# Kernel optimization log

Hardware: AMD Instinct MI355X
Metric: run time of the kernel (lower is better)

Reference implementation:

```python
import jax, jax.numpy as jnp
import numpy as np

SRC_LEN, TRG_LEN, BATCH, HID_DIM, ATT_DIM = 256, 256, 32, 512, 128


def setup_inputs() -> dict:
    key = jax.random.key(0)
    k1, k2, k3, k4, k5, k6 = jax.random.split(key, 6)
    dec_out = jax.random.normal(k1, (TRG_LEN, BATCH, HID_DIM), dtype=jnp.float32)
    enc_outs = jax.random.normal(k2, (SRC_LEN, BATCH, HID_DIM), dtype=jnp.float32)
    # Linear weights (scaled like kaiming-ish init so tanh isn't saturated)
    W_s = jax.random.normal(k3, (ATT_DIM, HID_DIM), dtype=jnp.float32) / np.sqrt(HID_DIM)
    W_t = jax.random.normal(k4, (ATT_DIM, HID_DIM), dtype=jnp.float32) / np.sqrt(HID_DIM)
    b_t = jax.random.normal(k5, (ATT_DIM,), dtype=jnp.float32) * 0.01
    # v_a ~ U(-0.05, 0.05), shape (att_dim, 1) as in the torch module
    v_a = jax.random.uniform(k6, (ATT_DIM, 1), dtype=jnp.float32, minval=-0.05, maxval=0.05)
    return {"dec_out": dec_out, "enc_outs": enc_outs, "W_s": W_s, "W_t": W_t, "b_t": b_t, "v_a": v_a}


def reference(dec_out, enc_outs, W_s, W_t, b_t, v_a):
    # enc projection: (src, batch, hid) -> (src, batch, att)
    enc_att = jnp.einsum('sbh,ah->sba', enc_outs, W_s)
    # dec projection (with bias): (trg, batch, hid) -> (trg, batch, att)
    dec_att = jnp.einsum('tbh,ah->tba', dec_out, W_t) + b_t
    # broadcast-add + tanh: (src, trg, batch, att), then reduce with v_a
    dec_enc = jnp.tanh(enc_att[:, None, :, :] + dec_att[None, :, :, :])
    scores = jnp.einsum('stba,a->tbs', dec_enc, v_a[:, 0])  # (trg, batch, src)
    return scores
```

## Files before the change

kernel.cpp:

```cpp
#include <hip/hip_runtime.h>

#define SRC_LEN 256
#define TRG_LEN 256
#define BATCH   32
#define HID     512
#define ATT     128
#define CSCALE  2.885390081777927f

typedef float  f32x4  __attribute__((ext_vector_type(4)));
typedef short  bf16x8 __attribute__((ext_vector_type(8)));

__device__ inline unsigned short bfr(float x) {
    unsigned u = __builtin_bit_cast(unsigned, x);
    return (unsigned short)((u + 0x7fffu + ((u >> 16) & 1u)) >> 16);
}
__device__ inline unsigned pk2(float a, float b) {
    return (unsigned)bfr(a) | ((unsigned)bfr(b) << 16);
}

__global__ __launch_bounds__(512) void proj_mfma(
    const float* __restrict__ dec_out, const float* __restrict__ enc_outs,
    const float* __restrict__ W_s, const float* __restrict__ W_t,
    const float* __restrict__ b_t,
    float* __restrict__ encE, float* __restrict__ decD)
{
    __shared__ __align__(16) char smem[49152];
    char* aLb = smem;
    char* bLb = smem + 16384;

    const int tid   = threadIdx.x;
    const int blk   = blockIdx.x;
    const bool isDec = blk >= 128;
    const int bb    = blk & 31;
    const int r0    = ((isDec ? blk - 128 : blk) >> 5) * 64;
    const float* __restrict__ in = isDec ? dec_out : enc_outs;
    const float* __restrict__ W  = isDec ? W_t : W_s;

    const int lane   = tid & 63;
    const int w      = tid >> 6;
    const int woff_m = (w & 3) * 16;
    const int woff_n = (w >> 2) * 64;
    const int q      = lane >> 4;
    const int l15    = lane & 15;
    const int l7     = lane & 7;

    const int srow = tid >> 4;
    const int skc  = tid & 15;
    const int sg   = skc >> 1, shalf = skc & 1;
    const float* aGp = in + ((size_t)(r0 + srow) * BATCH + bb) * HID + skc * 4;
    const float* wGp = W + (size_t)srow * HID + skc * 4;

    float4 aR[2];
    float4 wR[4];

    f32x4 acc[4];
    #pragma unroll
    for (int ni = 0; ni < 4; ++ni) acc[ni] = (f32x4)0.0f;

    #define LOADG(c)                                                          \
        {                                                                     \
            _Pragma("unroll")                                                 \
            for (int it = 0; it < 2; ++it)                                    \
                aR[it] = *(const float4*)(aGp + (size_t)it * 32 * BATCH * HID \
                                          + (c) * 64);                        \
            _Pragma("unroll")                                                 \
            for (int it = 0; it < 4; ++it)                                    \
                wR[it] = *(const float4*)(wGp + (size_t)it * 32 * HID         \
                                          + (c) * 64);                        \
        }

    #define STORES(buf)                                                      \
        {                                                                    \
            char* ab = aLb + (buf) * 8192;                                   \
            _Pragma("unroll")                                                \
            for (int it = 0; it < 2; ++it) {                                 \
                const int i = srow + it * 32;                                \
                uint2 u;                                                     \
                u.x = pk2(aR[it].x, aR[it].y);                               \
                u.y = pk2(aR[it].z, aR[it].w);                               \
                *(uint2*)(ab + i * 128 + ((sg ^ (i & 7)) << 4)               \
                          + shalf * 8) = u;                                  \
            }                                                                \
            char* bp = bLb + (buf) * 16384;                                  \
            _Pragma("unroll")                                                \
            for (int it = 0; it < 4; ++it) {                                 \
                const int rw = srow + it * 32;                               \
                uint2 u;                                                     \
                u.x = pk2(wR[it].x, wR[it].y);                               \
                u.y = pk2(wR[it].z, wR[it].w);                               \
                *(uint2*)(bp + rw * 128 + ((sg ^ (rw & 7)) << 4)             \
                          + shalf * 8) = u;                                  \
            }                                                                \
        }

    LOADG(0);
    STORES(0);
    __syncthreads();

    for (int c = 0; c < 8; ++c) {
        if (c < 7) LOADG(c + 1);
        const char* ab = aLb + (c & 1) * 8192;
        const char* bp = bLb + (c & 1) * 16384;
        #pragma unroll
        for (int s = 0; s < 2; ++s) {
            const int sw = ((s * 4 + q) ^ l7) * 16;
            bf16x8 af = *(const bf16x8*)(ab + (woff_m + l15) * 128 + sw);
            bf16x8 bfv[4];
            #pragma unroll
            for (int ni = 0; ni < 4; ++ni)
                bfv[ni] = *(const bf16x8*)(bp + (woff_n + ni * 16 + l15) * 128 + sw);
            #pragma unroll
            for (int ni = 0; ni < 4; ++ni)
                acc[ni] = __builtin_amdgcn_mfma_f32_16x16x32_bf16(
                    af, bfv[ni], acc[ni], 0, 0, 0);
        }
        if (c < 7) STORES((c + 1) & 1);
        __syncthreads();
    }

    if (!isDec) {
        float* T = (float*)smem;
        #pragma unroll
        for (int ni = 0; ni < 4; ++ni)
            #pragma unroll
            for (int r = 0; r < 4; ++r) {
                const int ml = woff_m + q * 4 + r;
                const int nl = woff_n + ni * 16 + l15;
                T[ml * 132 + nl] = __builtin_amdgcn_exp2f(-CSCALE * acc[ni][r]);
            }
        __syncthreads();
        {
            const int m  = tid & 63;
            const int g0 = tid >> 6;
            #pragma unroll
            for (int p = 0; p < 4; ++p) {
                const int gq = g0 + p * 8;
                float4 v = *(const float4*)(T + m * 132 + gq * 4);
                *(float4*)(encE + (((size_t)bb * 32 + gq) * SRC_LEN + r0 + m) * 4) = v;
            }
        }
    } else {
        float bt[4];
        #pragma unroll
        for (int ni = 0; ni < 4; ++ni) bt[ni] = b_t[woff_n + ni * 16 + l15];
        #pragma unroll
        for (int ni = 0; ni < 4; ++ni)
            #pragma unroll
            for (int r = 0; r < 4; ++r) {
                const int ml = woff_m + q * 4 + r;
                const int nl = woff_n + ni * 16 + l15;
                decD[((size_t)(r0 + ml) * BATCH + bb) * ATT + nl] =
                    __builtin_amdgcn_exp2f(CSCALE * (acc[ni][r] + bt[ni]));
            }
    }
    #undef LOADG
    #undef STORES
}

__global__ __launch_bounds__(256) void score_kernel(
    const float* __restrict__ encE, const float* __restrict__ decD,
    const float* __restrict__ v_a, float* __restrict__ out)
{
    __shared__ float dS[4 * ATT];
    __shared__ float vS[ATT];
    __shared__ float sumvS;

    const int tid = threadIdx.x;
    const int t0  = blockIdx.x * 4;
    const int b   = blockIdx.y;

    if (tid < 128) {
        const int tt = tid >> 5, a4 = (tid & 31) * 4;
        *(float4*)(dS + tt * ATT + a4) =
            *(const float4*)(decD + ((size_t)(t0 + tt) * BATCH + b) * ATT + a4);
    } else if (tid < 160) {
        const int l = tid - 128;
        *(float4*)(vS + l * 4) = *(const float4*)(v_a + l * 4);
    }
    __syncthreads();
    if (tid < 64) {
        float x = vS[tid] + vS[tid + 64];
        #pragma unroll
        for (int o = 32; o > 0; o >>= 1) x += __shfl_down(x, o);
        if (tid == 0) sumvS = x;
    }
    __syncthreads();

    float acc0 = 0.f, acc1 = 0.f, acc2 = 0.f, acc3 = 0.f;
    const float* __restrict__ ep = encE + ((size_t)b * 32 * SRC_LEN + tid) * 4;

    #pragma unroll
    for (int g = 0; g < 32; ++g) {
        const float4 E  = *(const float4*)(ep + (size_t)g * SRC_LEN * 4);
        const float4 vv = *(const float4*)(vS + g * 4);
        const float n0 = vv.x * E.x, n1 = vv.y * E.y;
        const float n2 = vv.z * E.z, n3 = vv.w * E.w;

        #define TSTEP(ACC, DBASE)                                          \
        {                                                                  \
            const float4 d = *(const float4*)(DBASE + g * 4);              \
            const float x0 = E.x + d.x, x1 = E.y + d.y;                    \
            const float x2 = E.z + d.z, x3 = E.w + d.w;                    \
            const float a01 = x0 * x1, a23 = x2 * x3;                      \
            const float den = a01 * a23;                                   \
            const float m01 = fmaf(n0, x1, n1 * x0);                       \
            const float m23 = fmaf(n2, x3, n3 * x2);                       \
            const float num = fmaf(m01, a23, m23 * a01);                   \
            ACC = fmaf(num, __builtin_amdgcn_rcpf(den), ACC);              \
        }
        TSTEP(acc0, dS + 0 * ATT)
        TSTEP(acc1, dS + 1 * ATT)
        TSTEP(acc2, dS + 2 * ATT)
        TSTEP(acc3, dS + 3 * ATT)
        #undef TSTEP
    }

    const float sv = sumvS;
    out[((size_t)(t0 + 0) * BATCH + b) * SRC_LEN + tid] = sv - 2.0f * acc0;
    out[((size_t)(t0 + 1) * BATCH + b) * SRC_LEN + tid] = sv - 2.0f * acc1;
    out[((size_t)(t0 + 2) * BATCH + b) * SRC_LEN + tid] = sv - 2.0f * acc2;
    out[((size_t)(t0 + 3) * BATCH + b) * SRC_LEN + tid] = sv - 2.0f * acc3;
}

extern "C" void kernel_launch(void* const* d_in, const int* in_sizes, int n_in,
                              void* d_out, int out_size, void* d_ws, size_t ws_size,
                              hipStream_t stream) {
    const float* dec_out  = (const float*)d_in[0];
    const float* enc_outs = (const float*)d_in[1];
    const float* W_s      = (const float*)d_in[2];
    const float* W_t      = (const float*)d_in[3];
    const float* b_t      = (const float*)d_in[4];
    const float* v_a      = (const float*)d_in[5];
    float* out = (float*)d_out;

    float* encE = (float*)d_ws;
    float* decD = encE + (size_t)BATCH * ATT * SRC_LEN;

    proj_mfma<<<256, 512, 0, stream>>>(dec_out, enc_outs, W_s, W_t, b_t, encE, decD);

    dim3 g3(TRG_LEN / 4, BATCH);
    score_kernel<<<g3, 256, 0, stream>>>(encE, decD, v_a, out);
}
```

Measured before the change: 116.5 us.

## Halve projection tiles, pack score math into float2, remap score grid

After: 118.5 us. No clear change (+1.7%).

```diff
diff --git a/kernel.cpp b/kernel.cpp
--- a/kernel.cpp
+++ b/kernel.cpp
@@ -8,6 +8,7 @@
 #define CSCALE  2.885390081777927f
 
 typedef float  f32x4  __attribute__((ext_vector_type(4)));
+typedef float  f32x2  __attribute__((ext_vector_type(2)));
 typedef short  bf16x8 __attribute__((ext_vector_type(8)));
 
 __device__ inline unsigned short bfr(float x) {
@@ -18,28 +19,29 @@
     return (unsigned)bfr(a) | ((unsigned)bfr(b) << 16);
 }
 
-__global__ __launch_bounds__(512) void proj_mfma(
+__global__ __launch_bounds__(512, 4) void proj_mfma(
     const float* __restrict__ dec_out, const float* __restrict__ enc_outs,
     const float* __restrict__ W_s, const float* __restrict__ W_t,
     const float* __restrict__ b_t,
     float* __restrict__ encE, float* __restrict__ decD)
 {
-    __shared__ __align__(16) char smem[49152];
+    __shared__ __align__(16) char smem[40960];
     char* aLb = smem;
-    char* bLb = smem + 16384;
+    char* bLb = smem + 8192;
 
     const int tid   = threadIdx.x;
     const int blk   = blockIdx.x;
-    const bool isDec = blk >= 128;
-    const int bb    = blk & 31;
-    const int r0    = ((isDec ? blk - 128 : blk) >> 5) * 64;
+    const bool isDec = blk >= 256;
+    const int blkL  = isDec ? blk - 256 : blk;
+    const int bb    = blkL & 31;
+    const int r0    = (blkL >> 5) * 32;
     const float* __restrict__ in = isDec ? dec_out : enc_outs;
     const float* __restrict__ W  = isDec ? W_t : W_s;
 
     const int lane   = tid & 63;
     const int w      = tid >> 6;
-    const int woff_m = (w & 3) * 16;
-    const int woff_n = (w >> 2) * 64;
+    const int woff_m = (w & 1) * 16;
+    const int woff_n = (w >> 1) * 32;
     const int q      = lane >> 4;
     const int l15    = lane & 15;
     const int l7     = lane & 7;
@@ -50,19 +52,16 @@
     const float* aGp = in + ((size_t)(r0 + srow) * BATCH + bb) * HID + skc * 4;
     const float* wGp = W + (size_t)srow * HID + skc * 4;
 
-    float4 aR[2];
+    float4 aR;
     float4 wR[4];
 
-    f32x4 acc[4];
-    #pragma unroll
-    for (int ni = 0; ni < 4; ++ni) acc[ni] = (f32x4)0.0f;
+    f32x4 acc[2];
+    acc[0] = (f32x4)0.0f;
+    acc[1] = (f32x4)0.0f;
 
     #define LOADG(c)                                                          \
         {                                                                     \
-            _Pragma("unroll")                                                 \
-            for (int it = 0; it < 2; ++it)                                    \
-                aR[it] = *(const float4*)(aGp + (size_t)it * 32 * BATCH * HID \
-                                          + (c) * 64);                        \
+            aR = *(const float4*)(aGp + (size_t)(c) * 64);                    \
             _Pragma("unroll")                                                 \
             for (int it = 0; it < 4; ++it)                                    \
                 wR[it] = *(const float4*)(wGp + (size_t)it * 32 * HID         \
@@ -71,13 +70,12 @@
 
     #define STORES(buf)                                                      \
         {                                                                    \
-            char* ab = aLb + (buf) * 8192;                                   \
-            _Pragma("unroll")                                                \
-            for (int it = 0; it < 2; ++it) {                                 \
-                const int i = srow + it * 32;                                \
+            char* ab = aLb + (buf) * 4096;                                   \
+            {                                                                \
+                const int i = srow;                                          \
                 uint2 u;                                                     \
-                u.x = pk2(aR[it].x, aR[it].y);                               \
-                u.y = pk2(aR[it].z, aR[it].w);                               \
+                u.x = pk2(aR.x, aR.y);                                       \
+                u.y = pk2(aR.z, aR.w);                                       \
                 *(uint2*)(ab + i * 128 + ((sg ^ (i & 7)) << 4)               \
                           + shalf * 8) = u;                                  \
             }                                                                \
@@ -99,18 +97,18 @@
 
     for (int c = 0; c < 8; ++c) {
         if (c < 7) LOADG(c + 1);
-        const char* ab = aLb + (c & 1) * 8192;
+        const char* ab = aLb + (c & 1) * 4096;
         const char* bp = bLb + (c & 1) * 16384;
         #pragma unroll
         for (int s = 0; s < 2; ++s) {
             const int sw = ((s * 4 + q) ^ l7) * 16;
             bf16x8 af = *(const bf16x8*)(ab + (woff_m + l15) * 128 + sw);
-            bf16x8 bfv[4];
-            #pragma unroll
-            for (int ni = 0; ni < 4; ++ni)
+            bf16x8 bfv[2];
+            #pragma unroll
+            for (int ni = 0; ni < 2; ++ni)
                 bfv[ni] = *(const bf16x8*)(bp + (woff_n + ni * 16 + l15) * 128 + sw);
             #pragma unroll
-            for (int ni = 0; ni < 4; ++ni)
+            for (int ni = 0; ni < 2; ++ni)
                 acc[ni] = __builtin_amdgcn_mfma_f32_16x16x32_bf16(
                     af, bfv[ni], acc[ni], 0, 0, 0);
         }
@@ -121,7 +119,7 @@
     if (!isDec) {
         float* T = (float*)smem;
         #pragma unroll
-        for (int ni = 0; ni < 4; ++ni)
+        for (int ni = 0; ni < 2; ++ni)
             #pragma unroll
             for (int r = 0; r < 4; ++r) {
                 const int ml = woff_m + q * 4 + r;
@@ -130,21 +128,21 @@
             }
         __syncthreads();
         {
-            const int m  = tid & 63;
-            const int g0 = tid >> 6;
-            #pragma unroll
-            for (int p = 0; p < 4; ++p) {
-                const int gq = g0 + p * 8;
+            const int m  = tid & 31;
+            const int g0 = tid >> 5;
+            #pragma unroll
+            for (int p = 0; p < 2; ++p) {
+                const int gq = g0 + p * 16;
                 float4 v = *(const float4*)(T + m * 132 + gq * 4);
                 *(float4*)(encE + (((size_t)bb * 32 + gq) * SRC_LEN + r0 + m) * 4) = v;
             }
         }
     } else {
-        float bt[4];
-        #pragma unroll
-        for (int ni = 0; ni < 4; ++ni) bt[ni] = b_t[woff_n + ni * 16 + l15];
-        #pragma unroll
-        for (int ni = 0; ni < 4; ++ni)
+        float bt[2];
+        bt[0] = b_t[woff_n + l15];
+        bt[1] = b_t[woff_n + 16 + l15];
+        #pragma unroll
+        for (int ni = 0; ni < 2; ++ni)
             #pragma unroll
             for (int r = 0; r < 4; ++r) {
                 const int ml = woff_m + q * 4 + r;
@@ -161,20 +159,26 @@
     const float* __restrict__ encE, const float* __restrict__ decD,
     const float* __restrict__ v_a, float* __restrict__ out)
 {
-    __shared__ float dS[4 * ATT];
+    __shared__ __align__(16) float dPf[2][ATT][2];
     __shared__ float vS[ATT];
     __shared__ float sumvS;
 
     const int tid = threadIdx.x;
-    const int t0  = blockIdx.x * 4;
-    const int b   = blockIdx.y;
-
-    if (tid < 128) {
-        const int tt = tid >> 5, a4 = (tid & 31) * 4;
-        *(float4*)(dS + tt * ATT + a4) =
-            *(const float4*)(decD + ((size_t)(t0 + tt) * BATCH + b) * ATT + a4);
-    } else if (tid < 160) {
-        const int l = tid - 128;
+    const int p   = blockIdx.x;
+    const int b   = (p & 7) * 4 + ((p >> 3) >> 6);
+    const int t0  = ((p >> 3) & 63) * 4;
+
+    if (tid < 64) {
+        const int pr = tid >> 5, a4 = (tid & 31) * 4;
+        const float4 dA = *(const float4*)(decD + ((size_t)(t0 + 2 * pr) * BATCH + b) * ATT + a4);
+        const float4 dB = *(const float4*)(decD + ((size_t)(t0 + 2 * pr + 1) * BATCH + b) * ATT + a4);
+        f32x2* dst = (f32x2*)&dPf[pr][a4][0];
+        dst[0] = (f32x2){dA.x, dB.x};
+        dst[1] = (f32x2){dA.y, dB.y};
+        dst[2] = (f32x2){dA.z, dB.z};
+        dst[3] = (f32x2){dA.w, dB.w};
+    } else if (tid < 96) {
+        const int l = tid - 64;
         *(float4*)(vS + l * 4) = *(const float4*)(v_a + l * 4);
     }
     __syncthreads();
@@ -186,40 +190,44 @@
     }
     __syncthreads();
 
-    float acc0 = 0.f, acc1 = 0.f, acc2 = 0.f, acc3 = 0.f;
+    f32x2 acc0 = {0.f, 0.f};
+    f32x2 acc1 = {0.f, 0.f};
     const float* __restrict__ ep = encE + ((size_t)b * 32 * SRC_LEN + tid) * 4;
+
+    #define PSTEP(ACC, PR)                                                 \
+    {                                                                      \
+        const f32x2* dp = (const f32x2*)&dPf[PR][g * 4][0];                \
+        const f32x2 x0 = e0 + dp[0], x1 = e1 + dp[1];                      \
+        const f32x2 x2 = e2 + dp[2], x3 = e3 + dp[3];                      \
+        const f32x2 a01 = x0 * x1, a23 = x2 * x3;                          \
+        const f32x2 den = a01 * a23;                                       \
+        const f32x2 m01 = n0 * x1 + n1 * x0;                               \
+        const f32x2 m23 = n2 * x3 + n3 * x2;                               \
+        const f32x2 num = m01 * a23 + m23 * a01;                           \
+        f32x2 r;                                                           \
+        r[0] = __builtin_amdgcn_rcpf(den[0]);                              \
+        r[1] = __builtin_amdgcn_rcpf(den[1]);                              \
+        ACC += num * r;                                                    \
+    }
 
     #pragma unroll
     for (int g = 0; g < 32; ++g) {
         const float4 E  = *(const float4*)(ep + (size_t)g * SRC_LEN * 4);
         const float4 vv = *(const float4*)(vS + g * 4);
-        const float n0 = vv.x * E.x, n1 = vv.y * E.y;
-        const float n2 = vv.z * E.z, n3 = vv.w * E.w;
-
-        #define TSTEP(ACC, DBASE)                                          \
-        {                                                                  \
-            const float4 d = *(const float4*)(DBASE + g * 4);              \
-            const float x0 = E.x + d.x, x1 = E.y + d.y;                    \
-            const float x2 = E.z + d.z, x3 = E.w + d.w;                    \
-            const float a01 = x0 * x1, a23 = x2 * x3;                      \
-            const float den = a01 * a23;                                   \
-            const float m01 = fmaf(n0, x1, n1 * x0);                       \
-            const float m23 = fmaf(n2, x3, n3 * x2);                       \
-            const float num = fmaf(m01, a23, m23 * a01);                   \
-            ACC = fmaf(num, __builtin_amdgcn_rcpf(den), ACC);              \
-        }
-        TSTEP(acc0, dS + 0 * ATT)
-        TSTEP(acc1, dS + 1 * ATT)
-        TSTEP(acc2, dS + 2 * ATT)
-        TSTEP(acc3, dS + 3 * ATT)
-        #undef TSTEP
-    }
+        const f32x2 e0 = {E.x, E.x}, e1 = {E.y, E.y};
+        const f32x2 e2 = {E.z, E.z}, e3 = {E.w, E.w};
+        const f32x2 n0 = vv.x * e0, n1 = vv.y * e1;
+        const f32x2 n2 = vv.z * e2, n3 = vv.w * e3;
+        PSTEP(acc0, 0)
+        PSTEP(acc1, 1)
+    }
+    #undef PSTEP
 
     const float sv = sumvS;
-    out[((size_t)(t0 + 0) * BATCH + b) * SRC_LEN + tid] = sv - 2.0f * acc0;
-    out[((size_t)(t0 + 1) * BATCH + b) * SRC_LEN + tid] = sv - 2.0f * acc1;
-    out[((size_t)(t0 + 2) * BATCH + b) * SRC_LEN + tid] = sv - 2.0f * acc2;
-    out[((size_t)(t0 + 3) * BATCH + b) * SRC_LEN + tid] = sv - 2.0f * acc3;
+    out[((size_t)(t0 + 0) * BATCH + b) * SRC_LEN + tid] = sv - 2.0f * acc0[0];
+    out[((size_t)(t0 + 1) * BATCH + b) * SRC_LEN + tid] = sv - 2.0f * acc0[1];
+    out[((size_t)(t0 + 2) * BATCH + b) * SRC_LEN + tid] = sv - 2.0f * acc1[0];
+    out[((size_t)(t0 + 3) * BATCH + b) * SRC_LEN + tid] = sv - 2.0f * acc1[1];
 }
 
 extern "C" void kernel_launch(void* const* d_in, const int* in_sizes, int n_in,
@@ -236,8 +244,7 @@
     float* encE = (float*)d_ws;
     float* decD = encE + (size_t)BATCH * ATT * SRC_LEN;
 
-    proj_mfma<<<256, 512, 0, stream>>>(dec_out, enc_outs, W_s, W_t, b_t, encE, decD);
-
-    dim3 g3(TRG_LEN / 4, BATCH);
-    score_kernel<<<g3, 256, 0, stream>>>(encE, decD, v_a, out);
-}
+    proj_mfma<<<512, 512, 0, stream>>>(dec_out, enc_outs, W_s, W_t, b_t, encE, decD);
+
+    score_kernel<<<2048, 256, 0, stream>>>(encE, decD, v_a, out);
+}
```

## Prepack bf16 weights in a prep kernel and shrink projection tiles

Applied to the files above, without the earlier changes.

New measurement: 123.1 us. 1.06x slower.

```diff
diff --git a/kernel.cpp b/kernel.cpp
--- a/kernel.cpp
+++ b/kernel.cpp
@@ -18,79 +18,81 @@
     return (unsigned)bfr(a) | ((unsigned)bfr(b) << 16);
 }
 
-__global__ __launch_bounds__(512) void proj_mfma(
+__global__ __launch_bounds__(256) void prep_kernel(
+    const float* __restrict__ W_s, const float* __restrict__ W_t,
+    const float* __restrict__ v_a,
+    uint4* __restrict__ Wb, float* __restrict__ sumvP)
+{
+    const int blk = blockIdx.x;
+    if (blk < 16) {
+        const int iw = blk >> 3, a_tile = blk & 7;
+        const float* __restrict__ W = iw ? W_t : W_s;
+        uint4* __restrict__ dst = Wb + ((size_t)iw * 8 + a_tile) * 1024;
+        #pragma unroll
+        for (int oo = 0; oo < 4; ++oo) {
+            const int o = threadIdx.x + oo * 256;
+            const int c = o >> 7, rem = o & 127;
+            const int s = rem >> 6, lane = rem & 63;
+            const int q = lane >> 4, l15 = lane & 15;
+            const int row = a_tile * 16 + l15;
+            const int k0 = c * 64 + s * 32 + q * 8;
+            const float4 f0 = *(const float4*)(W + (size_t)row * HID + k0);
+            const float4 f1 = *(const float4*)(W + (size_t)row * HID + k0 + 4);
+            uint4 u;
+            u.x = pk2(f0.x, f0.y); u.y = pk2(f0.z, f0.w);
+            u.z = pk2(f1.x, f1.y); u.w = pk2(f1.z, f1.w);
+            dst[o] = u;
+        }
+    } else {
+        const int tid = threadIdx.x;
+        float x = 0.f;
+        if (tid < 64) x = v_a[tid] + v_a[tid + 64];
+        #pragma unroll
+        for (int o = 32; o > 0; o >>= 1) x += __shfl_down(x, o);
+        if (tid == 0) *sumvP = x;
+    }
+}
+
+__global__ __launch_bounds__(256, 4) void proj_mfma(
     const float* __restrict__ dec_out, const float* __restrict__ enc_outs,
-    const float* __restrict__ W_s, const float* __restrict__ W_t,
-    const float* __restrict__ b_t,
+    const float* __restrict__ b_t, const uint4* __restrict__ Wb,
     float* __restrict__ encE, float* __restrict__ decD)
 {
-    __shared__ __align__(16) char smem[49152];
-    char* aLb = smem;
-    char* bLb = smem + 16384;
+    __shared__ __align__(16) char smem[8704];
 
     const int tid   = threadIdx.x;
     const int blk   = blockIdx.x;
-    const bool isDec = blk >= 128;
-    const int bb    = blk & 31;
-    const int r0    = ((isDec ? blk - 128 : blk) >> 5) * 64;
+    const bool isDec = blk >= 512;
+    const int blkL  = isDec ? blk - 512 : blk;
+    const int bb    = blkL & 31;
+    const int r0    = (blkL >> 5) * 16;
     const float* __restrict__ in = isDec ? dec_out : enc_outs;
-    const float* __restrict__ W  = isDec ? W_t : W_s;
-
-    const int lane   = tid & 63;
-    const int w      = tid >> 6;
-    const int woff_m = (w & 3) * 16;
-    const int woff_n = (w >> 2) * 64;
-    const int q      = lane >> 4;
-    const int l15    = lane & 15;
-    const int l7     = lane & 7;
+    const uint4* __restrict__ Wk = Wb + (isDec ? 8192 : 0);
+
+    const int lane = tid & 63;
+    const int w    = tid >> 6;
+    const int woff_n = w * 32;
+    const int q = lane >> 4, l15 = lane & 15, l7 = lane & 7;
 
     const int srow = tid >> 4;
     const int skc  = tid & 15;
     const int sg   = skc >> 1, shalf = skc & 1;
     const float* aGp = in + ((size_t)(r0 + srow) * BATCH + bb) * HID + skc * 4;
-    const float* wGp = W + (size_t)srow * HID + skc * 4;
-
-    float4 aR[2];
-    float4 wR[4];
-
-    f32x4 acc[4];
-    #pragma unroll
-    for (int ni = 0; ni < 4; ++ni) acc[ni] = (f32x4)0.0f;
-
-    #define LOADG(c)                                                          \
-        {                                                                     \
-            _Pragma("unroll")                                                 \
-            for (int it = 0; it < 2; ++it)                                    \
-                aR[it] = *(const float4*)(aGp + (size_t)it * 32 * BATCH * HID \
-                                          + (c) * 64);                        \
-            _Pragma("unroll")                                                 \
-            for (int it = 0; it < 4; ++it)                                    \
-                wR[it] = *(const float4*)(wGp + (size_t)it * 32 * HID         \
-                                          + (c) * 64);                        \
-        }
-
+
+    float4 aR;
+    f32x4 acc[2];
+    acc[0] = (f32x4)0.0f;
+    acc[1] = (f32x4)0.0f;
+
+    #define LOADG(c) { aR = *(const float4*)(aGp + (size_t)(c) * 64); }
     #define STORES(buf)                                                      \
         {                                                                    \
-            char* ab = aLb + (buf) * 8192;                                   \
-            _Pragma("unroll")                                                \
-            for (int it = 0; it < 2; ++it) {                                 \
-                const int i = srow + it * 32;                                \
-                uint2 u;                                                     \
-                u.x = pk2(aR[it].x, aR[it].y);                               \
-                u.y = pk2(aR[it].z, aR[it].w);                               \
-                *(uint2*)(ab + i * 128 + ((sg ^ (i & 7)) << 4)               \
-                          + shalf * 8) = u;                                  \
-            }                                                                \
-            char* bp = bLb + (buf) * 16384;                                  \
-            _Pragma("unroll")                                                \
-            for (int it = 0; it < 4; ++it) {                                 \
-                const int rw = srow + it * 32;                               \
-                uint2 u;                                                     \
-                u.x = pk2(wR[it].x, wR[it].y);                               \
-                u.y = pk2(wR[it].z, wR[it].w);                               \
-                *(uint2*)(bp + rw * 128 + ((sg ^ (rw & 7)) << 4)             \
-                          + shalf * 8) = u;                                  \
-            }                                                                \
+            char* ab = smem + (buf) * 2048;                                  \
+            uint2 u;                                                         \
+            u.x = pk2(aR.x, aR.y);                                           \
+            u.y = pk2(aR.z, aR.w);                                           \
+            *(uint2*)(ab + srow * 128 + ((sg ^ (srow & 7)) << 4)             \
+                      + shalf * 8) = u;                                      \
         }
 
     LOADG(0);
@@ -99,20 +101,18 @@
 
     for (int c = 0; c < 8; ++c) {
         if (c < 7) LOADG(c + 1);
-        const char* ab = aLb + (c & 1) * 8192;
-        const char* bp = bLb + (c & 1) * 16384;
+        const char* ab = smem + (c & 1) * 2048;
         #pragma unroll
         for (int s = 0; s < 2; ++s) {
-            const int sw = ((s * 4 + q) ^ l7) * 16;
-            bf16x8 af = *(const bf16x8*)(ab + (woff_m + l15) * 128 + sw);
-            bf16x8 bfv[4];
-            #pragma unroll
-            for (int ni = 0; ni < 4; ++ni)
-                bfv[ni] = *(const bf16x8*)(bp + (woff_n + ni * 16 + l15) * 128 + sw);
-            #pragma unroll
-            for (int ni = 0; ni < 4; ++ni)
+            bf16x8 af = *(const bf16x8*)(ab + l15 * 128
+                                         + (((s * 4 + q) ^ l7) << 4));
+            #pragma unroll
+            for (int ni = 0; ni < 2; ++ni) {
+                const int a_tile = w * 2 + ni;
+                bf16x8 bfv = *(const bf16x8*)(Wk + (((a_tile * 8 + c) * 2 + s) * 64 + lane));
                 acc[ni] = __builtin_amdgcn_mfma_f32_16x16x32_bf16(
-                    af, bfv[ni], acc[ni], 0, 0, 0);
+                    af, bfv, acc[ni], 0, 0, 0);
+            }
         }
         if (c < 7) STORES((c + 1) & 1);
         __syncthreads();
@@ -121,33 +121,33 @@
     if (!isDec) {
         float* T = (float*)smem;
         #pragma unroll
-        for (int ni = 0; ni < 4; ++ni)
+        for (int ni = 0; ni < 2; ++ni)
             #pragma unroll
             for (int r = 0; r < 4; ++r) {
-                const int ml = woff_m + q * 4 + r;
+                const int ml = q * 4 + r;
                 const int nl = woff_n + ni * 16 + l15;
                 T[ml * 132 + nl] = __builtin_amdgcn_exp2f(-CSCALE * acc[ni][r]);
             }
         __syncthreads();
         {
-            const int m  = tid & 63;
-            const int g0 = tid >> 6;
-            #pragma unroll
-            for (int p = 0; p < 4; ++p) {
-                const int gq = g0 + p * 8;
+            const int m  = tid & 15;
+            const int g0 = tid >> 4;
+            #pragma unroll
+            for (int p = 0; p < 2; ++p) {
+                const int gq = g0 + p * 16;
                 float4 v = *(const float4*)(T + m * 132 + gq * 4);
                 *(float4*)(encE + (((size_t)bb * 32 + gq) * SRC_LEN + r0 + m) * 4) = v;
             }
         }
     } else {
-        float bt[4];
-        #pragma unroll
-        for (int ni = 0; ni < 4; ++ni) bt[ni] = b_t[woff_n + ni * 16 + l15];
-        #pragma unroll
-        for (int ni = 0; ni < 4; ++ni)
+        float bt[2];
+        bt[0] = b_t[woff_n + l15];
+        bt[1] = b_t[woff_n + 16 + l15];
+        #pragma unroll
+        for (int ni = 0; ni < 2; ++ni)
             #pragma unroll
             for (int r = 0; r < 4; ++r) {
-                const int ml = woff_m + q * 4 + r;
+                const int ml = q * 4 + r;
                 const int nl = woff_n + ni * 16 + l15;
                 decD[((size_t)(r0 + ml) * BATCH + bb) * ATT + nl] =
                     __builtin_amdgcn_exp2f(CSCALE * (acc[ni][r] + bt[ni]));
@@ -159,46 +159,28 @@
 
 __global__ __launch_bounds__(256) void score_kernel(
     const float* __restrict__ encE, const float* __restrict__ decD,
-    const float* __restrict__ v_a, float* __restrict__ out)
+    const float* __restrict__ v_a, const float* __restrict__ sumvP,
+    float* __restrict__ out)
 {
-    __shared__ float dS[4 * ATT];
-    __shared__ float vS[ATT];
-    __shared__ float sumvS;
-
     const int tid = threadIdx.x;
     const int t0  = blockIdx.x * 4;
     const int b   = blockIdx.y;
 
-    if (tid < 128) {
-        const int tt = tid >> 5, a4 = (tid & 31) * 4;
-        *(float4*)(dS + tt * ATT + a4) =
-            *(const float4*)(decD + ((size_t)(t0 + tt) * BATCH + b) * ATT + a4);
-    } else if (tid < 160) {
-        const int l = tid - 128;
-        *(float4*)(vS + l * 4) = *(const float4*)(v_a + l * 4);
-    }
-    __syncthreads();
-    if (tid < 64) {
-        float x = vS[tid] + vS[tid + 64];
-        #pragma unroll
-        for (int o = 32; o > 0; o >>= 1) x += __shfl_down(x, o);
-        if (tid == 0) sumvS = x;
-    }
-    __syncthreads();
-
     float acc0 = 0.f, acc1 = 0.f, acc2 = 0.f, acc3 = 0.f;
     const float* __restrict__ ep = encE + ((size_t)b * 32 * SRC_LEN + tid) * 4;
+    const float* __restrict__ dBase = decD + ((size_t)t0 * BATCH + b) * ATT;
 
     #pragma unroll
     for (int g = 0; g < 32; ++g) {
         const float4 E  = *(const float4*)(ep + (size_t)g * SRC_LEN * 4);
-        const float4 vv = *(const float4*)(vS + g * 4);
+        const float4 vv = *(const float4*)(v_a + g * 4);
         const float n0 = vv.x * E.x, n1 = vv.y * E.y;
         const float n2 = vv.z * E.z, n3 = vv.w * E.w;
 
-        #define TSTEP(ACC, DBASE)                                          \
+        #define TSTEP(ACC, TT)                                             \
         {                                                                  \
-            const float4 d = *(const float4*)(DBASE + g * 4);              \
+            const float4 d = *(const float4*)(dBase                        \
+                + (size_t)(TT) * BATCH * ATT + g * 4);         \
             const float x0 = E.x + d.x, x1 = E.y + d.y;                    \
             const float x2 = E.z + d.z, x3 = E.w + d.w;                    \
             const float a01 = x0 * x1, a23 = x2 * x3;                      \
@@ -208,14 +190,14 @@
             const float num = fmaf(m01, a23, m23 * a01);                   \
             ACC = fmaf(num, __builtin_amdgcn_rcpf(den), ACC);              \
         }
-        TSTEP(acc0, dS + 0 * ATT)
-        TSTEP(acc1, dS + 1 * ATT)
-        TSTEP(acc2, dS + 2 * ATT)
-        TSTEP(acc3, dS + 3 * ATT)
+        TSTEP(acc0, 0)
+        TSTEP(acc1, 1)
+        TSTEP(acc2, 2)
+        TSTEP(acc3, 3)
         #undef TSTEP
     }
 
-    const float sv = sumvS;
+    const float sv = *sumvP;
     out[((size_t)(t0 + 0) * BATCH + b) * SRC_LEN + tid] = sv - 2.0f * acc0;
     out[((size_t)(t0 + 1) * BATCH + b) * SRC_LEN + tid] = sv - 2.0f * acc1;
     out[((size_t)(t0 + 2) * BATCH + b) * SRC_LEN + tid] = sv - 2.0f * acc2;
@@ -235,9 +217,10 @@
 
     float* encE = (float*)d_ws;
     float* decD = encE + (size_t)BATCH * ATT * SRC_LEN;
-
-    proj_mfma<<<256, 512, 0, stream>>>(dec_out, enc_outs, W_s, W_t, b_t, encE, decD);
-
-    dim3 g3(TRG_LEN / 4, BATCH);
-    score_kernel<<<g3, 256, 0, stream>>>(encE, decD, v_a, out);
-}
+    uint4* Wb   = (uint4*)(decD + (size_t)TRG_LEN * BATCH * ATT);
+    float* sumvP = (float*)(Wb + 2 * 8192);
+
+    prep_kernel<<<17, 256, 0, stream>>>(W_s, W_t, v_a, Wb, sumvP);
+    proj_mfma<<<1024, 256, 0, stream>>>(dec_out, enc_outs, b_t, Wb, encE, decD);
+    score_kernel<<<dim3(TRG_LEN / 4, BATCH), 256, 0, stream>>>(encE, decD, v_a, sumvP, out);
+}
```

## Register-tile score kernel over 4 sources x 4 targets per thread

Applied to the files above, without the earlier changes.

New measurement: 128.2 us. 10.1% more time.

```diff
diff --git a/kernel.cpp b/kernel.cpp
--- a/kernel.cpp
+++ b/kernel.cpp
@@ -161,22 +161,25 @@
     const float* __restrict__ encE, const float* __restrict__ decD,
     const float* __restrict__ v_a, float* __restrict__ out)
 {
-    __shared__ float dS[4 * ATT];
+    __shared__ __align__(16) float dS[16][ATT];
     __shared__ float vS[ATT];
     __shared__ float sumvS;
 
     const int tid = threadIdx.x;
-    const int t0  = blockIdx.x * 4;
+    const int t0  = blockIdx.x * 16;
     const int b   = blockIdx.y;
 
-    if (tid < 128) {
-        const int tt = tid >> 5, a4 = (tid & 31) * 4;
-        *(float4*)(dS + tt * ATT + a4) =
-            *(const float4*)(decD + ((size_t)(t0 + tt) * BATCH + b) * ATT + a4);
-    } else if (tid < 160) {
-        const int l = tid - 128;
-        *(float4*)(vS + l * 4) = *(const float4*)(v_a + l * 4);
-    }
+    {
+        const int tr0 = tid >> 5;
+        const int a4  = (tid & 31) * 4;
+        #pragma unroll
+        for (int p = 0; p < 2; ++p) {
+            const int tr = tr0 + p * 8;
+            *(float4*)(&dS[tr][a4]) =
+                *(const float4*)(decD + ((size_t)(t0 + tr) * BATCH + b) * ATT + a4);
+        }
+    }
+    if (tid < 32) *(float4*)(vS + tid * 4) = *(const float4*)(v_a + tid * 4);
     __syncthreads();
     if (tid < 64) {
         float x = vS[tid] + vS[tid + 64];
@@ -186,40 +189,57 @@
     }
     __syncthreads();
 
-    float acc0 = 0.f, acc1 = 0.f, acc2 = 0.f, acc3 = 0.f;
-    const float* __restrict__ ep = encE + ((size_t)b * 32 * SRC_LEN + tid) * 4;
-
+    const int w  = tid >> 6;
+    const int l  = tid & 63;
+    const int s0 = l * 4;
+
+    f32x4 acc[4];
     #pragma unroll
+    for (int i = 0; i < 4; ++i) acc[i] = (f32x4)0.0f;
+
+    const float* __restrict__ ep = encE + (size_t)b * 32 * SRC_LEN * 4 + s0 * 4;
+
+    #pragma unroll 4
     for (int g = 0; g < 32; ++g) {
-        const float4 E  = *(const float4*)(ep + (size_t)g * SRC_LEN * 4);
+        const float* epg = ep + (size_t)g * SRC_LEN * 4;
+        float4 E[4];
+        #pragma unroll
+        for (int si = 0; si < 4; ++si)
+            E[si] = *(const float4*)(epg + si * 4);
         const float4 vv = *(const float4*)(vS + g * 4);
-        const float n0 = vv.x * E.x, n1 = vv.y * E.y;
-        const float n2 = vv.z * E.z, n3 = vv.w * E.w;
-
-        #define TSTEP(ACC, DBASE)                                          \
-        {                                                                  \
-            const float4 d = *(const float4*)(DBASE + g * 4);              \
-            const float x0 = E.x + d.x, x1 = E.y + d.y;                    \
-            const float x2 = E.z + d.z, x3 = E.w + d.w;                    \
-            const float a01 = x0 * x1, a23 = x2 * x3;                      \
-            const float den = a01 * a23;                                   \
-            const float m01 = fmaf(n0, x1, n1 * x0);                       \
-            const float m23 = fmaf(n2, x3, n3 * x2);                       \
-            const float num = fmaf(m01, a23, m23 * a01);                   \
-            ACC = fmaf(num, __builtin_amdgcn_rcpf(den), ACC);              \
-        }
-        TSTEP(acc0, dS + 0 * ATT)
-        TSTEP(acc1, dS + 1 * ATT)
-        TSTEP(acc2, dS + 2 * ATT)
-        TSTEP(acc3, dS + 3 * ATT)
-        #undef TSTEP
+        float4 n[4];
+        #pragma unroll
+        for (int si = 0; si < 4; ++si) {
+            n[si].x = vv.x * E[si].x; n[si].y = vv.y * E[si].y;
+            n[si].z = vv.z * E[si].z; n[si].w = vv.w * E[si].w;
+        }
+        #pragma unroll
+        for (int i = 0; i < 4; ++i) {
+            const float4 d = *(const float4*)(&dS[w * 4 + i][g * 4]);
+            #pragma unroll
+            for (int si = 0; si < 4; ++si) {
+                const float x0 = E[si].x + d.x, x1 = E[si].y + d.y;
+                const float x2 = E[si].z + d.z, x3 = E[si].w + d.w;
+                const float a01 = x0 * x1, a23 = x2 * x3;
+                const float den = a01 * a23;
+                const float m01 = fmaf(n[si].x, x1, n[si].y * x0);
+                const float m23 = fmaf(n[si].z, x3, n[si].w * x2);
+                const float num = fmaf(m01, a23, m23 * a01);
+                acc[i][si] = fmaf(num, __builtin_amdgcn_rcpf(den), acc[i][si]);
+            }
+        }
     }
 
     const float sv = sumvS;
-    out[((size_t)(t0 + 0) * BATCH + b) * SRC_LEN + tid] = sv - 2.0f * acc0;
-    out[((size_t)(t0 + 1) * BATCH + b) * SRC_LEN + tid] = sv - 2.0f * acc1;
-    out[((size_t)(t0 + 2) * BATCH + b) * SRC_LEN + tid] = sv - 2.0f * acc2;
-    out[((size_t)(t0 + 3) * BATCH + b) * SRC_LEN + tid] = sv - 2.0f * acc3;
+    #pragma unroll
+    for (int i = 0; i < 4; ++i) {
+        float4 o;
+        o.x = sv - 2.0f * acc[i][0];
+        o.y = sv - 2.0f * acc[i][1];
+        o.z = sv - 2.0f * acc[i][2];
+        o.w = sv - 2.0f * acc[i][3];
+        *(float4*)(out + ((size_t)(t0 + w * 4 + i) * BATCH + b) * SRC_LEN + s0) = o;
+    }
 }
 
 extern "C" void kernel_launch(void* const* d_in, const int* in_sizes, int n_in,
@@ -238,6 +258,5 @@
 
     proj_mfma<<<256, 512, 0, stream>>>(dec_out, enc_outs, W_s, W_t, b_t, encE, decD);
 
-    dim3 g3(TRG_LEN / 4, BATCH);
-    score_kernel<<<g3, 256, 0, stream>>>(encE, decD, v_a, out);
-}
+    score_kernel<<<dim3(16, BATCH), 256, 0, stream>>>(encE, decD, v_a, out);
+}
```
